# Kernel tuning notes

Measured on AMD Instinct MI355X. Metric: run time of the kernel, lower is better.

## Reference

```python
import jax, jax.numpy as jnp
from jax import lax
import numpy as np

NUM_HEADS = 8


def setup_inputs() -> dict:
    key = jax.random.key(0)
    k1, k2, k3, k4, k5 = jax.random.split(key, 5)
    L, B, E = 512, 32, 512
    return {
        "query": jax.random.normal(k1, (L, B, E), dtype=jnp.float32),
        "in_proj_weight": jax.random.normal(k2, (3 * E, E, 3), dtype=jnp.float32) * (1.0 / np.sqrt(3 * E)),
        "in_proj_bias": jax.random.normal(k3, (3 * E,), dtype=jnp.float32) * 0.02,
        "attention_weight": jax.random.uniform(k4, (B, L, L), dtype=jnp.float32),
        "bpps": jax.random.uniform(k5, (B, L, L), dtype=jnp.float32),
    }


def reference(query, in_proj_weight, in_proj_bias, attention_weight, bpps):
    # Faithful port of the custom multi_head_attention_forward self-attention path.
    # NOTE: attention_weight and bpps are accepted by the original signature but
    # never used in its body; dropout_p=0 / eval mode; no out_proj exists.
    tgt_len, bsz, embed_dim = query.shape
    num_heads = NUM_HEADS
    head_dim = embed_dim // num_heads
    scaling = float(head_dim) ** -0.5

    # conv1d QKV projection: input (bsz, embed, len), kernel (3*embed, embed, 3), padding 1
    x = jnp.transpose(query, (1, 2, 0))  # (B, E, L)
    qkv = lax.conv_general_dilated(
        x, in_proj_weight, window_strides=(1,), padding=[(1, 1)],
        dimension_numbers=("NCH", "OIH", "NCH"))
    qkv = qkv + in_proj_bias[None, :, None]  # (B, 3E, L)
    q, k, v = jnp.split(qkv, 3, axis=1)  # each (B, E, L)

    def to_heads(t):
        # (B, E, L) -> (L, B, E) -> (L, B*H, hd) -> (B*H, L, hd)
        t = jnp.transpose(t, (2, 0, 1))
        return jnp.transpose(t.reshape(tgt_len, bsz * num_heads, head_dim), (1, 0, 2))

    q = to_heads(q) * scaling
    k = to_heads(k)
    v = to_heads(v)

    scores = jnp.einsum("btd,bsd->bts", q, k)  # (B*H, L, L)
    attn = jax.nn.softmax(scores, axis=-1)
    out = jnp.einsum("bts,bsd->btd", attn, v)  # (B*H, L, hd)

    attn_output = jnp.transpose(out, (1, 0, 2)).reshape(tgt_len, bsz, embed_dim)
    avg_weights = attn.reshape(bsz, num_heads, tgt_len, tgt_len).sum(axis=1) / num_heads
    return attn_output, avg_weights
```

## Files before the change

kernel.cpp:

```cpp
#include <hip/hip_runtime.h>
#include <hip/hip_bf16.h>

typedef __hip_bfloat16 bf16;
typedef __attribute__((ext_vector_type(8))) __bf16 bf16x8;
typedef __attribute__((ext_vector_type(4))) float f32x4;

__device__ __forceinline__ void gl16(const void* g, void* l) {
  __builtin_amdgcn_global_load_lds((__attribute__((address_space(1))) void*)g,
                                   (__attribute__((address_space(3))) void*)l, 16, 0, 0);
}
__device__ __forceinline__ bf16 f2b(float f) { return __float2bfloat16(f); }

__device__ __forceinline__ int swz(int row, int bytecol) {
  return bytecol ^ ((row & 7) << 4);
}

__global__ void __launch_bounds__(256) prep_x(const float* __restrict__ q, bf16* __restrict__ Xp) {
  int row = blockIdx.x;
  int b = row >> 9, l = row & 511;
  int t = threadIdx.x;
  float2 v = *(const float2*)(q + (size_t)l * 16384 + b * 512 + t * 2);
  __hip_bfloat162 o2; o2.x = f2b(v.x); o2.y = f2b(v.y);
  *(__hip_bfloat162*)(Xp + ((size_t)(b * 514 + l + 1)) * 512 + t * 2) = o2;
}

__global__ void __launch_bounds__(256) prep_w(const float* __restrict__ w, bf16* __restrict__ Wb) {
  int idx = blockIdx.x * 256 + threadIdx.x;
  int t = idx / 786432;
  int r = idx - t * 786432;
  int o = r >> 9, i = r & 511;
  Wb[idx] = f2b(w[(size_t)o * 1536 + i * 3 + t]);
}

__global__ void __launch_bounds__(256) conv_qkv(
    const bf16* __restrict__ Wb, const bf16* __restrict__ Xp,
    const float* __restrict__ bias,
    bf16* __restrict__ Qb, bf16* __restrict__ Kb, bf16* __restrict__ Vt) {
  __shared__ __align__(16) bf16 As[2][128 * 64];
  __shared__ __align__(16) bf16 Bs[2][128 * 64];
  const int tid = threadIdx.x;
  const int l0 = blockIdx.x * 128;
  const int o0 = blockIdx.y * 128;
  const int b  = blockIdx.z;
  const int lane = tid & 63, wid = tid >> 6;
  const int wm = (wid >> 1) * 64, wn = (wid & 1) * 64;
  const int lg = lane >> 4, lr = lane & 15;
  const int rsw = (lr & 7) << 4;

  f32x4 acc[4][4] = {};

  auto STAGE = [&](int step, int buf) {
    const int tap = step >> 3;
    const int k0 = (step & 7) * 64;
    const char* wbase = (const char*)Wb + ((size_t)tap * 786432 + (size_t)o0 * 512 + k0) * 2;
    const char* xbase = (const char*)Xp + (((size_t)(b * 514 + l0 + tap)) * 512 + k0) * 2;
    #pragma unroll
    for (int it = 0; it < 4; ++it) {
      int ofs = tid * 16 + it * 4096;
      int row = ofs >> 7, bc = swz(row, ofs & 127);
      gl16(wbase + (size_t)row * 1024 + bc, (char*)&As[buf][0] + ofs);
    }
    #pragma unroll
    for (int it = 0; it < 4; ++it) {
      int ofs = tid * 16 + it * 4096;
      int row = ofs >> 7, bc = swz(row, ofs & 127);
      gl16(xbase + (size_t)row * 1024 + bc, (char*)&Bs[buf][0] + ofs);
    }
  };

  STAGE(0, 0);
  int cur = 0;
  for (int step = 0; step < 24; ++step) {
    __syncthreads();
    if (step < 23) STAGE(step + 1, cur ^ 1);
    #pragma unroll
    for (int kk = 0; kk < 2; ++kk) {
      const int rcol = (kk * 64 + lg * 16) ^ rsw;
      bf16x8 a[4], bb[4];
      #pragma unroll
      for (int i = 0; i < 4; ++i)
        a[i] = *(const bf16x8*)((const char*)&As[cur][0] + (wm + i * 16 + lr) * 128 + rcol);
      #pragma unroll
      for (int j = 0; j < 4; ++j)
        bb[j] = *(const bf16x8*)((const char*)&Bs[cur][0] + (wn + j * 16 + lr) * 128 + rcol);
      #pragma unroll
      for (int i = 0; i < 4; ++i)
        #pragma unroll
        for (int j = 0; j < 4; ++j)
          acc[i][j] = __builtin_amdgcn_mfma_f32_16x16x32_bf16(a[i], bb[j], acc[i][j], 0, 0, 0);
    }
    cur ^= 1;
  }

  const int part = o0 >> 9;
  #pragma unroll
  for (int i = 0; i < 4; ++i) {
    #pragma unroll
    for (int j = 0; j < 4; ++j) {
      int mbase = o0 + wm + i * 16 + lg * 4;
      int l = l0 + wn + j * 16 + lr;
      #pragma unroll
      for (int r = 0; r < 4; ++r) {
        int o = mbase + r;
        float v = acc[i][j][r] + bias[o];
        int rem = o & 511;
        int h = rem >> 6, d = rem & 63;
        size_t bh = (size_t)(b * 8 + h);
        if (part == 0)      Qb[(bh * 512 + l) * 64 + d] = f2b(v * 0.125f);
        else if (part == 1) Kb[(bh * 512 + l) * 64 + d] = f2b(v);
        else                Vt[(bh * 64 + d) * 512 + l] = f2b(v);
      }
    }
  }
}

__global__ void __launch_bounds__(256) flash_fwd(
    const bf16* __restrict__ Qb, const bf16* __restrict__ Kb, const bf16* __restrict__ Vt,
    float* __restrict__ out0, float* __restrict__ m_arr, float* __restrict__ li_arr) {
  __shared__ __align__(16) bf16 Qs[64 * 64];
  __shared__ __align__(16) bf16 Ks[64 * 64];
  __shared__ __align__(16) bf16 Vs[64 * 64];
  __shared__ __align__(16) bf16 Ps[4][16 * 72];
  const int tid = threadIdx.x;
  const int t0 = blockIdx.x * 64;
  const int bh = blockIdx.y;
  const int b = bh >> 3, h = bh & 7;
  const int lane = tid & 63, w = tid >> 6;
  const int lg = lane >> 4, lr = lane & 15;
  const int rsw = (lr & 7) << 4;

  #pragma unroll
  for (int it = 0; it < 2; ++it) {
    int ofs = tid * 16 + it * 4096;
    int row = ofs >> 7, bc = swz(row, ofs & 127);
    gl16((const char*)(Qb + ((size_t)bh * 512 + t0 + row) * 64) + bc, (char*)Qs + ofs);
  }

  float mreg[4] = {-1e30f, -1e30f, -1e30f, -1e30f};
  float lreg[4] = {0.f, 0.f, 0.f, 0.f};
  f32x4 oacc[4] = {};

  for (int sc = 0; sc < 8; ++sc) {
    __syncthreads();
    #pragma unroll
    for (int it = 0; it < 2; ++it) {
      int ofs = tid * 16 + it * 4096;
      int row = ofs >> 7, bc = swz(row, ofs & 127);
      gl16((const char*)(Kb + ((size_t)bh * 512 + sc * 64 + row) * 64) + bc, (char*)Ks + ofs);
      gl16((const char*)(Vt + ((size_t)bh * 64 + row) * 512 + sc * 64) + bc, (char*)Vs + ofs);
    }
    __syncthreads();

    bf16x8 aq[2];
    #pragma unroll
    for (int kk = 0; kk < 2; ++kk)
      aq[kk] = *(const bf16x8*)((const char*)Qs + (w * 16 + lr) * 128 + ((kk * 64 + lg * 16) ^ rsw));

    f32x4 s4[4] = {};
    #pragma unroll
    for (int j = 0; j < 4; ++j)
      #pragma unroll
      for (int kk = 0; kk < 2; ++kk) {
        bf16x8 bk = *(const bf16x8*)((const char*)Ks + (j * 16 + lr) * 128 + ((kk * 64 + lg * 16) ^ rsw));
        s4[j] = __builtin_amdgcn_mfma_f32_16x16x32_bf16(aq[kk], bk, s4[j], 0, 0, 0);
      }

    float cm[4], mnew[4], alpha[4], rs[4];
    #pragma unroll
    for (int r = 0; r < 4; ++r) {
      cm[r] = fmaxf(fmaxf(s4[0][r], s4[1][r]), fmaxf(s4[2][r], s4[3][r]));
      cm[r] = fmaxf(cm[r], __shfl_xor(cm[r], 1, 64));
      cm[r] = fmaxf(cm[r], __shfl_xor(cm[r], 2, 64));
      cm[r] = fmaxf(cm[r], __shfl_xor(cm[r], 4, 64));
      cm[r] = fmaxf(cm[r], __shfl_xor(cm[r], 8, 64));
      mnew[r] = fmaxf(mreg[r], cm[r]);
      alpha[r] = __expf(mreg[r] - mnew[r]);
      rs[r] = 0.f;
    }
    #pragma unroll
    for (int j = 0; j < 4; ++j)
      #pragma unroll
      for (int r = 0; r < 4; ++r) {
        float p = __expf(s4[j][r] - mnew[r]);
        s4[j][r] = p;
        rs[r] += p;
      }
    #pragma unroll
    for (int r = 0; r < 4; ++r) {
      rs[r] += __shfl_xor(rs[r], 1, 64);
      rs[r] += __shfl_xor(rs[r], 2, 64);
      rs[r] += __shfl_xor(rs[r], 4, 64);
      rs[r] += __shfl_xor(rs[r], 8, 64);
      lreg[r] = lreg[r] * alpha[r] + rs[r];
      mreg[r] = mnew[r];
    }
    #pragma unroll
    for (int j = 0; j < 4; ++j)
      #pragma unroll
      for (int r = 0; r < 4; ++r)
        oacc[j][r] *= alpha[r];

    #pragma unroll
    for (int j = 0; j < 4; ++j)
      #pragma unroll
      for (int r = 0; r < 4; ++r)
        Ps[w][(lg * 4 + r) * 72 + j * 16 + lr] = f2b(s4[j][r]);
    asm volatile("s_waitcnt lgkmcnt(0)" ::: "memory");
    __builtin_amdgcn_sched_barrier(0);

    bf16x8 pa[2];
    #pragma unroll
    for (int kk = 0; kk < 2; ++kk)
      pa[kk] = *(const bf16x8*)((const char*)&Ps[w][0] + lr * 144 + kk * 64 + lg * 16);

    #pragma unroll
    for (int j = 0; j < 4; ++j)
      #pragma unroll
      for (int kk = 0; kk < 2; ++kk) {
        bf16x8 bv = *(const bf16x8*)((const char*)Vs + (j * 16 + lr) * 128 + ((kk * 64 + lg * 16) ^ rsw));
        oacc[j] = __builtin_amdgcn_mfma_f32_16x16x32_bf16(pa[kk], bv, oacc[j], 0, 0, 0);
      }
  }

  float il[4];
  #pragma unroll
  for (int r = 0; r < 4; ++r) il[r] = 1.f / lreg[r];

  #pragma unroll
  for (int j = 0; j < 4; ++j)
    #pragma unroll
    for (int r = 0; r < 4; ++r) {
      int t = t0 + w * 16 + lg * 4 + r;
      out0[(size_t)t * 16384 + (size_t)b * 512 + h * 64 + j * 16 + lr] = oacc[j][r] * il[r];
    }
  if (lr == 0) {
    #pragma unroll
    for (int r = 0; r < 4; ++r) {
      int t = t0 + w * 16 + lg * 4 + r;
      m_arr[bh * 512 + t] = mreg[r];
      li_arr[bh * 512 + t] = il[r];
    }
  }
}

__global__ void __launch_bounds__(256) avg_attn(
    const bf16* __restrict__ Qb, const bf16* __restrict__ Kb,
    const float* __restrict__ m_arr, const float* __restrict__ li_arr,
    float* __restrict__ out1) {
  __shared__ __align__(16) bf16 Qs[64 * 64];
  __shared__ __align__(16) bf16 Ks[128 * 64];
  const int tid = threadIdx.x;
  const int s0 = blockIdx.x * 128;
  const int t0 = blockIdx.y * 64;
  const int b  = blockIdx.z;
  const int lane = tid & 63, w = tid >> 6;
  const int lg = lane >> 4, lr = lane & 15;
  const int rsw = (lr & 7) << 4;

  f32x4 avg4[8] = {};

  for (int h = 0; h < 8; ++h) {
    int bh = b * 8 + h;
    __syncthreads();
    #pragma unroll
    for (int it = 0; it < 2; ++it) {
      int ofs = tid * 16 + it * 4096;
      int row = ofs >> 7, bc = swz(row, ofs & 127);
      gl16((const char*)(Qb + ((size_t)bh * 512 + t0 + row) * 64) + bc, (char*)Qs + ofs);
    }
    #pragma unroll
    for (int it = 0; it < 4; ++it) {
      int ofs = tid * 16 + it * 4096;
      int row = ofs >> 7, bc = swz(row, ofs & 127);
      gl16((const char*)(Kb + ((size_t)bh * 512 + s0 + row) * 64) + bc, (char*)Ks + ofs);
    }
    __syncthreads();

    float mv[4], iv[4];
    #pragma unroll
    for (int r = 0; r < 4; ++r) {
      int t = t0 + w * 16 + lg * 4 + r;
      mv[r] = m_arr[bh * 512 + t];
      iv[r] = li_arr[bh * 512 + t];
    }

    bf16x8 aq[2];
    #pragma unroll
    for (int kk = 0; kk < 2; ++kk)
      aq[kk] = *(const bf16x8*)((const char*)Qs + (w * 16 + lr) * 128 + ((kk * 64 + lg * 16) ^ rsw));

    #pragma unroll
    for (int j = 0; j < 8; ++j) {
      f32x4 s4 = {};
      #pragma unroll
      for (int kk = 0; kk < 2; ++kk) {
        bf16x8 bk = *(const bf16x8*)((const char*)Ks + (j * 16 + lr) * 128 + ((kk * 64 + lg * 16) ^ rsw));
        s4 = __builtin_amdgcn_mfma_f32_16x16x32_bf16(aq[kk], bk, s4, 0, 0, 0);
      }
      #pragma unroll
      for (int r = 0; r < 4; ++r)
        avg4[j][r] += __expf(s4[r] - mv[r]) * iv[r];
    }
  }

  #pragma unroll
  for (int j = 0; j < 8; ++j)
    #pragma unroll
    for (int r = 0; r < 4; ++r) {
      int t = t0 + w * 16 + lg * 4 + r;
      out1[((size_t)b * 512 + t) * 512 + s0 + j * 16 + lr] = avg4[j][r] * 0.125f;
    }
}

extern "C" void kernel_launch(void* const* d_in, const int* in_sizes, int n_in,
                              void* d_out, int out_size, void* d_ws, size_t ws_size,
                              hipStream_t stream) {
  const float* query = (const float*)d_in[0];
  const float* wconv = (const float*)d_in[1];
  const float* bias  = (const float*)d_in[2];

  char* ws = (char*)d_ws;
  bf16* Xp  = (bf16*)(ws + 0);
  bf16* Wb  = (bf16*)(ws + 16842752);
  bf16* Qb  = (bf16*)(ws + 21561344);
  bf16* Kb  = (bf16*)(ws + 38338560);
  bf16* Vt  = (bf16*)(ws + 55115776);
  float* m_arr  = (float*)(ws + 71892992);
  float* li_arr = (float*)(ws + 72417280);

  float* out0 = (float*)d_out;
  float* out1 = out0 + 8388608;

  hipMemsetAsync(Xp, 0, 16842752, stream);
  prep_x<<<16384, 256, 0, stream>>>(query, Xp);
  prep_w<<<9216, 256, 0, stream>>>(wconv, Wb);
  conv_qkv<<<dim3(4, 12, 32), 256, 0, stream>>>(Wb, Xp, bias, Qb, Kb, Vt);
  flash_fwd<<<dim3(8, 256), 256, 0, stream>>>(Qb, Kb, Vt, out0, m_arr, li_arr);
  avg_attn<<<dim3(4, 8, 32), 256, 0, stream>>>(Qb, Kb, m_arr, li_arr, out1);
}
```

Measured before the change: 363.4 us.

## Reuse one staged input tile across all three conv taps per K-chunk

The conv QKV GEMM now loops over 8 K-chunks instead of 24 tap×K steps. Each stage loads the three per-tap weight tiles plus a single 130-row input tile (padded to 136). Every tap then reads from the same input tile at a row offset, with the swizzle adjusted to match. This cuts repeated global loads of the input window and reduces the number of barriers. In exchange, LDS use per block grows to roughly 130KB, which likely limits each CU to one resident block and reduces latency hiding.

```diff
diff --git a/kernel.cpp b/kernel.cpp
--- a/kernel.cpp
+++ b/kernel.cpp
@@ -36,8 +36,8 @@
     const bf16* __restrict__ Wb, const bf16* __restrict__ Xp,
     const float* __restrict__ bias,
     bf16* __restrict__ Qb, bf16* __restrict__ Kb, bf16* __restrict__ Vt) {
-  __shared__ __align__(16) bf16 As[2][128 * 64];
-  __shared__ __align__(16) bf16 Bs[2][128 * 64];
+  __shared__ __align__(16) bf16 As[2][3][128 * 64];
+  __shared__ __align__(16) bf16 Bs[2][136 * 64];
   const int tid = threadIdx.x;
   const int l0 = blockIdx.x * 128;
   const int o0 = blockIdx.y * 128;
@@ -45,49 +45,61 @@
   const int lane = tid & 63, wid = tid >> 6;
   const int wm = (wid >> 1) * 64, wn = (wid & 1) * 64;
   const int lg = lane >> 4, lr = lane & 15;
-  const int rsw = (lr & 7) << 4;
 
   f32x4 acc[4][4] = {};
 
-  auto STAGE = [&](int step, int buf) {
-    const int tap = step >> 3;
-    const int k0 = (step & 7) * 64;
-    const char* wbase = (const char*)Wb + ((size_t)tap * 786432 + (size_t)o0 * 512 + k0) * 2;
-    const char* xbase = (const char*)Xp + (((size_t)(b * 514 + l0 + tap)) * 512 + k0) * 2;
+  auto STAGE = [&](int k0, int buf) {
+    const char* wb0 = (const char*)Wb + ((size_t)o0 * 512 + k0) * 2;
+    const char* xb0 = (const char*)Xp + (((size_t)(b * 514 + l0)) * 512 + k0) * 2;
+    #pragma unroll
+    for (int tap = 0; tap < 3; ++tap) {
+      const char* wt = wb0 + (size_t)tap * 1572864;
+      #pragma unroll
+      for (int it = 0; it < 4; ++it) {
+        int ofs = tid * 16 + it * 4096;
+        int row = ofs >> 7, bc = swz(row, ofs & 127);
+        gl16(wt + (size_t)row * 1024 + bc, (char*)&As[buf][tap][0] + ofs);
+      }
+    }
     #pragma unroll
     for (int it = 0; it < 4; ++it) {
       int ofs = tid * 16 + it * 4096;
       int row = ofs >> 7, bc = swz(row, ofs & 127);
-      gl16(wbase + (size_t)row * 1024 + bc, (char*)&As[buf][0] + ofs);
-    }
-    #pragma unroll
-    for (int it = 0; it < 4; ++it) {
-      int ofs = tid * 16 + it * 4096;
-      int row = ofs >> 7, bc = swz(row, ofs & 127);
-      gl16(xbase + (size_t)row * 1024 + bc, (char*)&Bs[buf][0] + ofs);
+      gl16(xb0 + (size_t)row * 1024 + bc, (char*)&Bs[buf][0] + ofs);
+    }
+    if (tid < 16) {
+      int row = 128 + (tid >> 3);
+      int bc  = swz(row, (tid & 7) * 16);
+      gl16(xb0 + (size_t)row * 1024 + bc, (char*)&Bs[buf][0] + 128 * 128 + tid * 16);
     }
   };
 
   STAGE(0, 0);
   int cur = 0;
-  for (int step = 0; step < 24; ++step) {
-    __syncthreads();
-    if (step < 23) STAGE(step + 1, cur ^ 1);
-    #pragma unroll
-    for (int kk = 0; kk < 2; ++kk) {
-      const int rcol = (kk * 64 + lg * 16) ^ rsw;
-      bf16x8 a[4], bb[4];
-      #pragma unroll
-      for (int i = 0; i < 4; ++i)
-        a[i] = *(const bf16x8*)((const char*)&As[cur][0] + (wm + i * 16 + lr) * 128 + rcol);
-      #pragma unroll
-      for (int j = 0; j < 4; ++j)
-        bb[j] = *(const bf16x8*)((const char*)&Bs[cur][0] + (wn + j * 16 + lr) * 128 + rcol);
-      #pragma unroll
-      for (int i = 0; i < 4; ++i)
+  for (int k0 = 0; k0 < 512; k0 += 64) {
+    __syncthreads();
+    if (k0 < 448) STAGE(k0 + 64, cur ^ 1);
+    #pragma unroll
+    for (int tap = 0; tap < 3; ++tap) {
+      const int rswA = (lr & 7) << 4;
+      const int rswB = ((lr + tap) & 7) << 4;
+      #pragma unroll
+      for (int kk = 0; kk < 2; ++kk) {
+        const int colA = (kk * 64 + lg * 16) ^ rswA;
+        const int colB = (kk * 64 + lg * 16) ^ rswB;
+        bf16x8 a[4], bb[4];
+        #pragma unroll
+        for (int i = 0; i < 4; ++i)
+          a[i] = *(const bf16x8*)((const char*)&As[cur][tap][0] + (wm + i * 16 + lr) * 128 + colA);
         #pragma unroll
         for (int j = 0; j < 4; ++j)
-          acc[i][j] = __builtin_amdgcn_mfma_f32_16x16x32_bf16(a[i], bb[j], acc[i][j], 0, 0, 0);
+          bb[j] = *(const bf16x8*)((const char*)&Bs[cur][0] + (wn + j * 16 + lr + tap) * 128 + colB);
+        #pragma unroll
+        for (int i = 0; i < 4; ++i)
+          #pragma unroll
+          for (int j = 0; j < 4; ++j)
+            acc[i][j] = __builtin_amdgcn_mfma_f32_16x16x32_bf16(a[i], bb[j], acc[i][j], 0, 0, 0);
+      }
     }
     cur ^= 1;
   }
```

New measurement: 351.8 us. 3.2% less time.
